# Optimization experiments

Measured on AMD Instinct MI355X. Metric: run time of the kernel, lower is better.

The kernel has to match this reference:

```python
import jax, jax.numpy as jnp
import numpy as np

D = 768      # hidden_size
H = 12       # num_head
HD = D // H  # head_dim
LN_EPS = 1e-5


def setup_inputs() -> dict:
    key = jax.random.key(0)
    ks = jax.random.split(key, 9)
    N, S = 4, 2048
    s = 0.02
    return {
        "hidden_state": jax.random.normal(ks[0], (N, S, D), dtype=jnp.float32),
        "key_padding_mask": jax.random.randint(ks[1], (N, S), 0, 2, dtype=jnp.int64),
        "Wq": jax.random.normal(ks[2], (D, D), dtype=jnp.float32) * s,
        "Wk": jax.random.normal(ks[3], (D, D), dtype=jnp.float32) * s,
        "Wv": jax.random.normal(ks[4], (D, D), dtype=jnp.float32) * s,
        "Wo": jax.random.normal(ks[5], (D, D), dtype=jnp.float32) * s,
        "W1": jax.random.normal(ks[6], (4 * D, D), dtype=jnp.float32) * s,
        "W2": jax.random.normal(ks[7], (D, 4 * D), dtype=jnp.float32) * s,
        "ln_g": jnp.ones((D,), dtype=jnp.float32),
        "ln_b": jnp.zeros((D,), dtype=jnp.float32),
    }


def _layernorm(x, g, b):
    mu = jnp.mean(x, axis=-1, keepdims=True)
    var = jnp.mean(jnp.square(x - mu), axis=-1, keepdims=True)
    return (x - mu) * jax.lax.rsqrt(var + LN_EPS) * g + b


def reference(hidden_state, key_padding_mask, Wq, Wk, Wv, Wo, W1, W2, ln_g, ln_b):
    x = hidden_state
    N, S, _ = x.shape
    # Note: original module projects K and V from `query` (self-attention).
    def proj(W):
        return (x @ W.T).reshape(N, S, H, HD).transpose(0, 2, 1, 3)  # [N,H,S,HD]
    Q, K, V = proj(Wq), proj(Wk), proj(Wv)
    scores = jnp.einsum("bhqd,bhkd->bhqk", Q, K)  # [N,H,S,S]
    # int mask: 0 marks padding positions -> masked with -inf
    pad = (key_padding_mask == 0)[:, None, None, :]  # [N,1,1,S]
    scores = jnp.where(pad, -jnp.inf, scores)
    attn = jax.nn.softmax(scores / np.sqrt(HD), axis=-1)
    ctx = jnp.einsum("bhqk,bhkd->bhqd", attn, V)
    ctx = ctx.transpose(0, 2, 1, 3).reshape(N, S, D)
    mha = ctx @ Wo.T
    # residual + LayerNorm (same LN params used twice, as in the original)
    n1 = _layernorm(x + mha, ln_g, ln_b)
    # FFN with exact GELU (torch nn.GELU default)
    f = jax.nn.gelu(n1 @ W1.T, approximate=False) @ W2.T
    return _layernorm(n1 + f, ln_g, ln_b)
```

## Files before the change

kernel.cpp:

```cpp
#include <hip/hip_runtime.h>
#include <math.h>

typedef unsigned short u16;
typedef unsigned int u32;
typedef __bf16 bf16x8 __attribute__((ext_vector_type(8)));
typedef float f32x4 __attribute__((ext_vector_type(4)));
typedef u32 u32x4 __attribute__((ext_vector_type(4)));

#define NB 4
#define SS 2048
#define DD 768
#define HH 12
#define HD 64
#define ROWS (NB*SS)

__device__ __forceinline__ u16 f2bf(float f) {
    union { float f; unsigned u; } v; v.f = f;
    unsigned r = v.u + 0x7fffu + ((v.u >> 16) & 1u);
    return (u16)(r >> 16);
}
__device__ __forceinline__ u32 fas(float f) { union { float f; u32 u; } v; v.f = f; return v.u; }

__device__ __forceinline__ void gl_lds16(const void* g, void* l) {
    __builtin_amdgcn_global_load_lds((__attribute__((address_space(1))) void*)(g),
                                     (__attribute__((address_space(3))) void*)(l),
                                     16, 0, 0);
}

__global__ __launch_bounds__(256) void prep_kernel(
        const float* __restrict__ X, const float* __restrict__ Wq,
        const float* __restrict__ Wk, const float* __restrict__ Wv,
        const float* __restrict__ Wo, const float* __restrict__ W1,
        const float* __restrict__ W2, const int* __restrict__ mask,
        u16* __restrict__ Xb, u16* __restrict__ Wqkvb, u16* __restrict__ Wob,
        u16* __restrict__ W1b, u16* __restrict__ W2b, float* __restrict__ mb) {
    const int blk = blockIdx.x, tid = threadIdx.x;
    const float* src; u16* dst; int idx;
    if (blk < 6144)       { src = X;  dst = Xb;               idx = blk * 1024 + tid * 4; }
    else if (blk < 6720)  { src = Wq; dst = Wqkvb;            idx = (blk - 6144) * 1024 + tid * 4; }
    else if (blk < 7296)  { src = Wk; dst = Wqkvb + DD * DD;  idx = (blk - 6720) * 1024 + tid * 4; }
    else if (blk < 7872)  { src = Wv; dst = Wqkvb + 2*DD*DD;  idx = (blk - 7296) * 1024 + tid * 4; }
    else if (blk < 8448)  { src = Wo; dst = Wob;              idx = (blk - 7872) * 1024 + tid * 4; }
    else if (blk < 10752) { src = W1; dst = W1b;              idx = (blk - 8448) * 1024 + tid * 4; }
    else if (blk < 13056) { src = W2; dst = W2b;              idx = (blk - 10752) * 1024 + tid * 4; }
    else {
        int i = (blk - 13056) * 1024 + tid * 4;
        float4 o;
        o.x = mask[i]     == 0 ? -1e30f : 0.0f;
        o.y = mask[i + 1] == 0 ? -1e30f : 0.0f;
        o.z = mask[i + 2] == 0 ? -1e30f : 0.0f;
        o.w = mask[i + 3] == 0 ? -1e30f : 0.0f;
        *(float4*)&mb[i] = o;
        return;
    }
    float4 v = *(const float4*)&src[idx];
    ushort4 o;
    o.x = f2bf(v.x); o.y = f2bf(v.y); o.z = f2bf(v.z); o.w = f2bf(v.w);
    *(ushort4*)&dst[idx] = o;
}

template <int EPI, int BN>
__global__ __launch_bounds__(256) void gemm_bt(const u16* __restrict__ A,
                                               const u16* __restrict__ B,
                                               int M, int N, int K,
                                               void* __restrict__ out,
                                               const void* __restrict__ aux,
                                               u16* __restrict__ Qb,
                                               u16* __restrict__ Kb,
                                               u16* __restrict__ Vb) {
    __shared__ __align__(16) u16 lA[128 * 64];
    __shared__ __align__(16) u16 lB[BN * 64];
    constexpr int MI = (BN == 128) ? 4 : 2;
    const int tid = threadIdx.x;
    const int lane = tid & 63, wave = tid >> 6;
    const int quad = lane >> 4, lc = lane & 15;
    const int xcd = blockIdx.x & 7, loc = blockIdx.x >> 3;
    const int mb = xcd * 8 + (loc & 7), nb = loc >> 3;
    const int m0 = mb * 128, n0 = nb * BN;
    const int wrow = (BN == 128) ? (wave >> 1) * 64 : wave * 32;
    const int wcol = (BN == 128) ? (wave & 1) * 64 : 0;
    const int swz = lc & 7;

    f32x4 acc[MI][4] = {};

    for (int kb = 0; kb < K; kb += 64) {
        __syncthreads();
#pragma unroll
        for (int p0 = 0; p0 < 1024; p0 += 256) {
            int p = p0 + tid, row = p >> 3, cl = (p & 7) ^ (row & 7);
            gl_lds16(A + (size_t)(m0 + row) * K + kb + cl * 8, &lA[(size_t)(p0 + wave * 64) * 8]);
        }
#pragma unroll
        for (int p0 = 0; p0 < BN * 8; p0 += 256) {
            int p = p0 + tid, row = p >> 3, cl = (p & 7) ^ (row & 7);
            gl_lds16(B + (size_t)(n0 + row) * K + kb + cl * 8, &lB[(size_t)(p0 + wave * 64) * 8]);
        }
        __syncthreads();
#pragma unroll
        for (int k2 = 0; k2 < 2; ++k2) {
            bf16x8 af[MI], bfr[4];
#pragma unroll
            for (int t = 0; t < MI; ++t)
                af[t] = *(const bf16x8*)&lA[(wrow + t * 16 + lc) * 64 + ((quad + k2 * 4) ^ swz) * 8];
#pragma unroll
            for (int t = 0; t < 4; ++t)
                bfr[t] = *(const bf16x8*)&lB[(wcol + t * 16 + lc) * 64 + ((quad + k2 * 4) ^ swz) * 8];
#pragma unroll
            for (int mi = 0; mi < MI; ++mi)
#pragma unroll
                for (int ni = 0; ni < 4; ++ni)
                    acc[mi][ni] = __builtin_amdgcn_mfma_f32_16x16x32_bf16(af[mi], bfr[ni],
                                                                         acc[mi][ni], 0, 0, 0);
        }
    }

#pragma unroll
    for (int mi = 0; mi < MI; ++mi) {
#pragma unroll
        for (int r = 0; r < 4; ++r) {
            int m = m0 + wrow + mi * 16 + quad * 4 + r;
#pragma unroll
            for (int ni = 0; ni < 4; ++ni) {
                int n = n0 + wcol + ni * 16 + lc;
                float v = acc[mi][ni][r];
                if constexpr (EPI == 0) {
                    int b = m >> 11, s = m & 2047;
                    int which = n / DD, rem = n - which * DD;
                    int h = rem >> 6, d = rem & 63;
                    u16* dst = which == 0 ? Qb : (which == 1 ? Kb : Vb);
                    dst[((((size_t)b * HH + h) * SS + s) << 6) + d] = f2bf(v);
                } else if constexpr (EPI == 1) {
                    float u = v * fmaf(v * v, 0.035677408f, 0.7978845608f);
                    float e = __builtin_amdgcn_exp2f(u * 2.885390082f);
                    float g = v - v * __builtin_amdgcn_rcpf(e + 1.0f);
                    ((u16*)out)[(size_t)m * N + n] = f2bf(g);
                } else if constexpr (EPI == 2) {
                    ((float*)out)[(size_t)m * N + n] =
                        v + ((const float*)aux)[(size_t)m * N + n];
                } else {
                    ((float*)out)[(size_t)m * N + n] =
                        v + (float)(((const __bf16*)aux)[(size_t)m * N + n]);
                }
            }
        }
    }
}

__global__ __launch_bounds__(256) void transpose_v(const u16* __restrict__ V,
                                                   u16* __restrict__ Vt) {
    __shared__ u16 t[32][33];
    int bh = blockIdx.z;
    int s0 = blockIdx.x * 32, d0 = blockIdx.y * 32;
    const u16* vb = V + (size_t)bh * SS * HD;
    u16* vtb = Vt + (size_t)bh * HD * SS;
    int tx = threadIdx.x & 31, ty = threadIdx.x >> 5;
#pragma unroll
    for (int i = 0; i < 32; i += 8) t[ty + i][tx] = vb[(size_t)(s0 + ty + i) * HD + d0 + tx];
    __syncthreads();
#pragma unroll
    for (int i = 0; i < 32; i += 8) vtb[(size_t)(d0 + ty + i) * SS + s0 + tx] = t[tx][ty + i];
}

__global__ __launch_bounds__(256, 3) void attn_kernel(const u16* __restrict__ Q,
                                                      const u16* __restrict__ K,
                                                      const u16* __restrict__ Vt,
                                                      const float* __restrict__ maskbias,
                                                      u16* __restrict__ Ctx) {
    __shared__ __align__(16) u16 lK[2][4224];
    __shared__ __align__(16) u16 lV[2][4096];
    const int tid = threadIdx.x, lane = tid & 63, wave = tid >> 6;
    const int quad = lane >> 4, lc = lane & 15;
    const int bh = blockIdx.x % (NB * HH);
    const int b = bh / HH, h = bh - b * HH;
    const int q0 = (blockIdx.x / (NB * HH)) * 128;
    const u16* Qg = Q + ((size_t)bh * SS + q0 + wave * 32) * HD;
    const u16* Kg = K + (size_t)bh * SS * HD;
    const u16* Vg = Vt + (size_t)bh * HD * SS;
    const float* mbg = maskbias + b * SS;
    const int sw = lc & 7;

    const int srow = tid >> 3, scl = (tid & 7) ^ (srow & 7);
    const int srow2 = (256 + tid) >> 3, scl2 = (tid & 7) ^ (srow2 & 7);

    auto stage = [&](int bi, int j0) {
        gl_lds16(Kg + (size_t)(j0 + srow) * HD + scl * 8,   &lK[bi][(size_t)(wave * 64) * 8]);
        gl_lds16(Kg + (size_t)(j0 + srow2) * HD + scl2 * 8, &lK[bi][(size_t)(256 + wave * 64) * 8]);
        gl_lds16(Vg + (size_t)srow * SS + j0 + scl * 8,     &lV[bi][(size_t)(wave * 64) * 8]);
        gl_lds16(Vg + (size_t)srow2 * SS + j0 + scl2 * 8,   &lV[bi][(size_t)(256 + wave * 64) * 8]);
        if (lane < 16) gl_lds16(mbg + j0 + lane * 4, &lK[bi][4096]);
    };

    bf16x8 qf[2][2];
#pragma unroll
    for (int mi = 0; mi < 2; ++mi)
#pragma unroll
        for (int k2 = 0; k2 < 2; ++k2)
            qf[mi][k2] = *(const bf16x8*)(Qg + (size_t)(mi * 16 + lc) * HD + k2 * 32 + quad * 8);

    bf16x8 onesf;
#pragma unroll
    for (int i = 0; i < 8; ++i) onesf[i] = (__bf16)1.0f;

    f32x4 oacc[2][4] = {};
    f32x4 lsum[2] = {};

    stage(0, 0);
    for (int t = 0; t < SS / 64; ++t) {
        const int cur = t & 1;
        if (t < SS / 64 - 1) {
            stage(cur ^ 1, (t + 1) * 64);
            __builtin_amdgcn_sched_barrier(0);
            asm volatile("s_waitcnt vmcnt(5)" ::: "memory");
        } else {
            __builtin_amdgcn_sched_barrier(0);
            asm volatile("s_waitcnt vmcnt(0)" ::: "memory");
        }
        __builtin_amdgcn_sched_barrier(0);
        __builtin_amdgcn_s_barrier();
        __builtin_amdgcn_sched_barrier(0);

        const u16* bK = &lK[cur][0];
        const u16* bV = &lV[cur][0];
        const float* bM = (const float*)&lK[cur][4096];

        f32x4 sacc[2][4] = {};
        __builtin_amdgcn_s_setprio(1);
#pragma unroll
        for (int k2 = 0; k2 < 2; ++k2) {
            bf16x8 kf[4];
#pragma unroll
            for (int ni = 0; ni < 4; ++ni)
                kf[ni] = *(const bf16x8*)&bK[(ni * 16 + lc) * 64 + ((quad + k2 * 4) ^ sw) * 8];
#pragma unroll
            for (int ni = 0; ni < 4; ++ni) {
                sacc[0][ni] = __builtin_amdgcn_mfma_f32_16x16x32_bf16(kf[ni], qf[0][k2], sacc[0][ni], 0, 0, 0);
                sacc[1][ni] = __builtin_amdgcn_mfma_f32_16x16x32_bf16(kf[ni], qf[1][k2], sacc[1][ni], 0, 0, 0);
            }
        }
        __builtin_amdgcn_s_setprio(0);

        u32 pa[2][4], pb[2][4];
#pragma unroll
        for (int ni = 0; ni < 4; ++ni) {
            f32x4 mbv = *(const f32x4*)&bM[ni * 16 + quad * 4];
#pragma unroll
            for (int mi = 0; mi < 2; ++mi) {
#pragma unroll
                for (int r = 0; r < 4; ++r)
                    sacc[mi][ni][r] = __builtin_amdgcn_exp2f(fmaf(sacc[mi][ni][r], 0.180336880f, mbv[r]));
                pa[mi][ni] = __builtin_amdgcn_perm(fas(sacc[mi][ni][1]), fas(sacc[mi][ni][0]), 0x07060302);
                pb[mi][ni] = __builtin_amdgcn_perm(fas(sacc[mi][ni][3]), fas(sacc[mi][ni][2]), 0x07060302);
            }
        }

        bf16x8 pf[2][2];
#pragma unroll
        for (int mi = 0; mi < 2; ++mi)
#pragma unroll
            for (int k2 = 0; k2 < 2; ++k2) {
                u32 xa = pa[mi][2 * k2], ya = pa[mi][2 * k2 + 1];
                u32 xb = pb[mi][2 * k2], yb = pb[mi][2 * k2 + 1];
                asm("v_permlane32_swap_b32 %0, %1" : "+v"(xa), "+v"(ya));
                asm("v_permlane16_swap_b32 %0, %1" : "+v"(xa), "+v"(ya));
                asm("v_permlane32_swap_b32 %0, %1" : "+v"(xb), "+v"(yb));
                asm("v_permlane16_swap_b32 %0, %1" : "+v"(xb), "+v"(yb));
                u32x4 pw = { xa, xb, ya, yb };
                pf[mi][k2] = __builtin_bit_cast(bf16x8, pw);
            }

        __builtin_amdgcn_s_setprio(1);
#pragma unroll
        for (int k2 = 0; k2 < 2; ++k2) {
            lsum[0] = __builtin_amdgcn_mfma_f32_16x16x32_bf16(pf[0][k2], onesf, lsum[0], 0, 0, 0);
            lsum[1] = __builtin_amdgcn_mfma_f32_16x16x32_bf16(pf[1][k2], onesf, lsum[1], 0, 0, 0);
#pragma unroll
            for (int ni = 0; ni < 4; ++ni) {
                bf16x8 vf = *(const bf16x8*)&bV[(ni * 16 + lc) * 64 + ((quad + k2 * 4) ^ sw) * 8];
                oacc[0][ni] = __builtin_amdgcn_mfma_f32_16x16x32_bf16(pf[0][k2], vf, oacc[0][ni], 0, 0, 0);
                oacc[1][ni] = __builtin_amdgcn_mfma_f32_16x16x32_bf16(pf[1][k2], vf, oacc[1][ni], 0, 0, 0);
            }
        }
        __builtin_amdgcn_s_setprio(0);

        __builtin_amdgcn_sched_barrier(0);
        __builtin_amdgcn_s_barrier();
    }

#pragma unroll
    for (int mi = 0; mi < 2; ++mi)
#pragma unroll
        for (int r = 0; r < 4; ++r) {
            float inv = 1.0f / lsum[mi][r];
            int s = q0 + wave * 32 + mi * 16 + quad * 4 + r;
            size_t base = ((size_t)(b * SS + s)) * DD + h * HD;
#pragma unroll
            for (int ni = 0; ni < 4; ++ni)
                Ctx[base + ni * 16 + lc] = f2bf(oacc[mi][ni][r] * inv);
        }
}

__global__ __launch_bounds__(256) void ln_kernel(const float* __restrict__ in,
                                                 const float* __restrict__ g,
                                                 const float* __restrict__ bb,
                                                 u16* __restrict__ out_bf,
                                                 float* __restrict__ out_f) {
    const int row = blockIdx.x, tid = threadIdx.x;
    const float* x = in + (size_t)row * DD;
    float v0 = x[tid], v1 = x[tid + 256], v2 = x[tid + 512];
    float s = v0 + v1 + v2;
    float q = v0 * v0 + v1 * v1 + v2 * v2;
#pragma unroll
    for (int o = 1; o < 64; o <<= 1) {
        s += __shfl_xor(s, o);
        q += __shfl_xor(q, o);
    }
    __shared__ float rs[4], rq[4];
    int wave = tid >> 6;
    if ((tid & 63) == 0) { rs[wave] = s; rq[wave] = q; }
    __syncthreads();
    s = rs[0] + rs[1] + rs[2] + rs[3];
    q = rq[0] + rq[1] + rq[2] + rq[3];
    float mu = s * (1.0f / DD);
    float var = q * (1.0f / DD) - mu * mu;
    float rstd = rsqrtf(var + 1e-5f);
#pragma unroll
    for (int j = 0; j < 3; ++j) {
        int col = tid + j * 256;
        float v = (j == 0 ? v0 : (j == 1 ? v1 : v2));
        float y = (v - mu) * rstd * g[col] + bb[col];
        if (out_bf) out_bf[(size_t)row * DD + col] = f2bf(y);
        if (out_f) out_f[(size_t)row * DD + col] = y;
    }
}

extern "C" void kernel_launch(void* const* d_in, const int* in_sizes, int n_in,
                              void* d_out, int out_size, void* d_ws, size_t ws_size,
                              hipStream_t stream) {
    const float* X    = (const float*)d_in[0];
    const int*   mask = (const int*)d_in[1];
    const float* Wq   = (const float*)d_in[2];
    const float* Wk   = (const float*)d_in[3];
    const float* Wv   = (const float*)d_in[4];
    const float* Wo   = (const float*)d_in[5];
    const float* W1   = (const float*)d_in[6];
    const float* W2   = (const float*)d_in[7];
    const float* ln_g = (const float*)d_in[8];
    const float* ln_b = (const float*)d_in[9];
    float* out = (float*)d_out;

    char* ws = (char*)d_ws;
    size_t off = 0;
    auto alloc = [&](size_t bytes) {
        void* p = ws + off;
        off += (bytes + 255) & ~(size_t)255;
        return p;
    };
    u16*   Xbf   = (u16*)alloc((size_t)ROWS * DD * 2);
    u16*   Wqkvb = (u16*)alloc((size_t)3 * DD * DD * 2);
    u16*   Wob   = (u16*)alloc((size_t)DD * DD * 2);
    u16*   W1b   = (u16*)alloc((size_t)4 * DD * DD * 2);
    u16*   W2b   = (u16*)alloc((size_t)4 * DD * DD * 2);
    float* mbias = (float*)alloc((size_t)NB * SS * 4);
    u16*   Qb    = (u16*)alloc((size_t)ROWS * DD * 2);
    u16*   Kb    = (u16*)alloc((size_t)ROWS * DD * 2);
    u16*   Vb    = (u16*)alloc((size_t)ROWS * DD * 2);
    u16*   Vtb   = (u16*)alloc((size_t)ROWS * DD * 2);
    float* resid = (float*)alloc((size_t)ROWS * DD * 4);
    u16*   n1b   = (u16*)alloc((size_t)ROWS * DD * 2);
    u16*   Gb    = Qb;
    u16*   Ctxb  = Xbf;
    float* h2    = resid;

    prep_kernel<<<dim3(13064), dim3(256), 0, stream>>>(
        X, Wq, Wk, Wv, Wo, W1, W2, mask,
        Xbf, Wqkvb, Wob, W1b, W2b, mbias);

    gemm_bt<0, 128><<<dim3((3 * DD / 128) * (ROWS / 128)), dim3(256), 0, stream>>>(
        Xbf, Wqkvb, ROWS, 3 * DD, DD, nullptr, nullptr, Qb, Kb, Vb);

    transpose_v<<<dim3(SS / 32, HD / 32, NB * HH), dim3(256), 0, stream>>>(Vb, Vtb);

    attn_kernel<<<dim3((SS / 128) * (NB * HH)), dim3(256), 0, stream>>>(
        Qb, Kb, Vtb, mbias, Ctxb);

    gemm_bt<2, 64><<<dim3((DD / 64) * (ROWS / 128)), dim3(256), 0, stream>>>(
        Ctxb, Wob, ROWS, DD, DD, resid, X, nullptr, nullptr, nullptr);

    ln_kernel<<<dim3(ROWS), dim3(256), 0, stream>>>(resid, ln_g, ln_b, n1b, nullptr);

    gemm_bt<1, 128><<<dim3((4 * DD / 128) * (ROWS / 128)), dim3(256), 0, stream>>>(
        n1b, W1b, ROWS, 4 * DD, DD, Gb, nullptr, nullptr, nullptr, nullptr);

    gemm_bt<3, 64><<<dim3((DD / 64) * (ROWS / 128)), dim3(256), 0, stream>>>(
        Gb, W2b, ROWS, DD, 4 * DD, h2, n1b, nullptr, nullptr, nullptr);

    ln_kernel<<<dim3(ROWS), dim3(256), 0, stream>>>(h2, ln_g, ln_b, nullptr, out);
}
```

Measured before the change: 354.4 us.

## Compact unmasked keys/values and skip padded key tiles in attention

Adds a per-batch prefix-scan kernel over the key padding mask that assigns compacted indices to non-padded positions. The QKV GEMM epilogue scatters K and V rows into these compacted slots, transpose_v skips tiles past the valid count, and attention loops only over ceil(count/64) key tiles, zeroing probabilities in the final partial tile. This removes the additive mask-bias loads and roughly halves attention work for a random 50% mask. It is an exact reformulation, at the cost of a small extra kernel and a scattered epilogue write.

```diff
diff --git a/kernel.cpp b/kernel.cpp
--- a/kernel.cpp
+++ b/kernel.cpp
@@ -31,9 +31,9 @@
         const float* __restrict__ X, const float* __restrict__ Wq,
         const float* __restrict__ Wk, const float* __restrict__ Wv,
         const float* __restrict__ Wo, const float* __restrict__ W1,
-        const float* __restrict__ W2, const int* __restrict__ mask,
+        const float* __restrict__ W2,
         u16* __restrict__ Xb, u16* __restrict__ Wqkvb, u16* __restrict__ Wob,
-        u16* __restrict__ W1b, u16* __restrict__ W2b, float* __restrict__ mb) {
+        u16* __restrict__ W1b, u16* __restrict__ W2b) {
     const int blk = blockIdx.x, tid = threadIdx.x;
     const float* src; u16* dst; int idx;
     if (blk < 6144)       { src = X;  dst = Xb;               idx = blk * 1024 + tid * 4; }
@@ -42,21 +42,45 @@
     else if (blk < 7872)  { src = Wv; dst = Wqkvb + 2*DD*DD;  idx = (blk - 7296) * 1024 + tid * 4; }
     else if (blk < 8448)  { src = Wo; dst = Wob;              idx = (blk - 7872) * 1024 + tid * 4; }
     else if (blk < 10752) { src = W1; dst = W1b;              idx = (blk - 8448) * 1024 + tid * 4; }
-    else if (blk < 13056) { src = W2; dst = W2b;              idx = (blk - 10752) * 1024 + tid * 4; }
-    else {
-        int i = (blk - 13056) * 1024 + tid * 4;
-        float4 o;
-        o.x = mask[i]     == 0 ? -1e30f : 0.0f;
-        o.y = mask[i + 1] == 0 ? -1e30f : 0.0f;
-        o.z = mask[i + 2] == 0 ? -1e30f : 0.0f;
-        o.w = mask[i + 3] == 0 ? -1e30f : 0.0f;
-        *(float4*)&mb[i] = o;
-        return;
-    }
+    else                  { src = W2; dst = W2b;              idx = (blk - 10752) * 1024 + tid * 4; }
     float4 v = *(const float4*)&src[idx];
     ushort4 o;
     o.x = f2bf(v.x); o.y = f2bf(v.y); o.z = f2bf(v.z); o.w = f2bf(v.w);
     *(ushort4*)&dst[idx] = o;
+}
+
+__global__ __launch_bounds__(256) void scan_kernel(const int* __restrict__ mask,
+                                                   int* __restrict__ cidx,
+                                                   int* __restrict__ cnt) {
+    const int b = blockIdx.x, tid = threadIdx.x;
+    const int lane = tid & 63, wave = tid >> 6;
+    const int base = b * SS + tid * 8;
+    int4 m0 = *(const int4*)&mask[base];
+    int4 m1 = *(const int4*)&mask[base + 4];
+    int v[8] = { m0.x != 0, m0.y != 0, m0.z != 0, m0.w != 0,
+                 m1.x != 0, m1.y != 0, m1.z != 0, m1.w != 0 };
+    int own = 0;
+#pragma unroll
+    for (int i = 0; i < 8; ++i) own += v[i];
+    int inc = own;
+#pragma unroll
+    for (int o = 1; o < 64; o <<= 1) {
+        int n = __shfl_up(inc, o);
+        if (lane >= o) inc += n;
+    }
+    __shared__ int wsum[4];
+    if (lane == 63) wsum[wave] = inc;
+    __syncthreads();
+    int wbase = 0;
+#pragma unroll
+    for (int w = 0; w < 4; ++w) wbase += (w < wave) ? wsum[w] : 0;
+    int pos = wbase + inc - own;
+    int o8[8];
+#pragma unroll
+    for (int i = 0; i < 8; ++i) { o8[i] = v[i] ? pos : -1; pos += v[i]; }
+    *(int4*)&cidx[base]     = make_int4(o8[0], o8[1], o8[2], o8[3]);
+    *(int4*)&cidx[base + 4] = make_int4(o8[4], o8[5], o8[6], o8[7]);
+    if (tid == 255) cnt[b] = wbase + inc;
 }
 
 template <int EPI, int BN>
@@ -67,7 +91,8 @@
                                                const void* __restrict__ aux,
                                                u16* __restrict__ Qb,
                                                u16* __restrict__ Kb,
-                                               u16* __restrict__ Vb) {
+                                               u16* __restrict__ Vb,
+                                               const int* __restrict__ cidx) {
     __shared__ __align__(16) u16 lA[128 * 64];
     __shared__ __align__(16) u16 lB[BN * 64];
     constexpr int MI = (BN == 128) ? 4 : 2;
@@ -116,6 +141,12 @@
 
 #pragma unroll
     for (int mi = 0; mi < MI; ++mi) {
+        int csa[4];
+        if constexpr (EPI == 0) {
+            int mbase = m0 + wrow + mi * 16 + quad * 4;
+            int4 cs4 = *(const int4*)&cidx[(mbase >> 11) * SS + (mbase & 2047)];
+            csa[0] = cs4.x; csa[1] = cs4.y; csa[2] = cs4.z; csa[3] = cs4.w;
+        }
 #pragma unroll
         for (int r = 0; r < 4; ++r) {
             int m = m0 + wrow + mi * 16 + quad * 4 + r;
@@ -128,7 +159,9 @@
                     int which = n / DD, rem = n - which * DD;
                     int h = rem >> 6, d = rem & 63;
                     u16* dst = which == 0 ? Qb : (which == 1 ? Kb : Vb);
-                    dst[((((size_t)b * HH + h) * SS + s) << 6) + d] = f2bf(v);
+                    int sidx = which == 0 ? s : csa[r];
+                    if (sidx >= 0)
+                        dst[((((size_t)b * HH + h) * SS + sidx) << 6) + d] = f2bf(v);
                 } else if constexpr (EPI == 1) {
                     float u = v * fmaf(v * v, 0.035677408f, 0.7978845608f);
                     float e = __builtin_amdgcn_exp2f(u * 2.885390082f);
@@ -147,15 +180,22 @@
 }
 
 __global__ __launch_bounds__(256) void transpose_v(const u16* __restrict__ V,
-                                                   u16* __restrict__ Vt) {
+                                                   u16* __restrict__ Vt,
+                                                   const int* __restrict__ cnt) {
     __shared__ u16 t[32][33];
     int bh = blockIdx.z;
+    int c = cnt[bh / HH];
+    int cr = (c + 63) & ~63;
     int s0 = blockIdx.x * 32, d0 = blockIdx.y * 32;
+    if (s0 >= cr) return;
     const u16* vb = V + (size_t)bh * SS * HD;
     u16* vtb = Vt + (size_t)bh * HD * SS;
     int tx = threadIdx.x & 31, ty = threadIdx.x >> 5;
 #pragma unroll
-    for (int i = 0; i < 32; i += 8) t[ty + i][tx] = vb[(size_t)(s0 + ty + i) * HD + d0 + tx];
+    for (int i = 0; i < 32; i += 8) {
+        int s = s0 + ty + i;
+        t[ty + i][tx] = (s < c) ? vb[(size_t)s * HD + d0 + tx] : (u16)0;
+    }
     __syncthreads();
 #pragma unroll
     for (int i = 0; i < 32; i += 8) vtb[(size_t)(d0 + ty + i) * SS + s0 + tx] = t[tx][ty + i];
@@ -164,9 +204,9 @@
 __global__ __launch_bounds__(256, 3) void attn_kernel(const u16* __restrict__ Q,
                                                       const u16* __restrict__ K,
                                                       const u16* __restrict__ Vt,
-                                                      const float* __restrict__ maskbias,
+                                                      const int* __restrict__ cntg,
                                                       u16* __restrict__ Ctx) {
-    __shared__ __align__(16) u16 lK[2][4224];
+    __shared__ __align__(16) u16 lK[2][4096];
     __shared__ __align__(16) u16 lV[2][4096];
     const int tid = threadIdx.x, lane = tid & 63, wave = tid >> 6;
     const int quad = lane >> 4, lc = lane & 15;
@@ -176,8 +216,9 @@
     const u16* Qg = Q + ((size_t)bh * SS + q0 + wave * 32) * HD;
     const u16* Kg = K + (size_t)bh * SS * HD;
     const u16* Vg = Vt + (size_t)bh * HD * SS;
-    const float* mbg = maskbias + b * SS;
     const int sw = lc & 7;
+    const int cnt = cntg[b];
+    const int nt = (cnt + 63) >> 6;
 
     const int srow = tid >> 3, scl = (tid & 7) ^ (srow & 7);
     const int srow2 = (256 + tid) >> 3, scl2 = (tid & 7) ^ (srow2 & 7);
@@ -187,7 +228,6 @@
         gl_lds16(Kg + (size_t)(j0 + srow2) * HD + scl2 * 8, &lK[bi][(size_t)(256 + wave * 64) * 8]);
         gl_lds16(Vg + (size_t)srow * SS + j0 + scl * 8,     &lV[bi][(size_t)(wave * 64) * 8]);
         gl_lds16(Vg + (size_t)srow2 * SS + j0 + scl2 * 8,   &lV[bi][(size_t)(256 + wave * 64) * 8]);
-        if (lane < 16) gl_lds16(mbg + j0 + lane * 4, &lK[bi][4096]);
     };
 
     bf16x8 qf[2][2];
@@ -205,12 +245,12 @@
     f32x4 lsum[2] = {};
 
     stage(0, 0);
-    for (int t = 0; t < SS / 64; ++t) {
+    for (int t = 0; t < nt; ++t) {
         const int cur = t & 1;
-        if (t < SS / 64 - 1) {
+        if (t < nt - 1) {
             stage(cur ^ 1, (t + 1) * 64);
             __builtin_amdgcn_sched_barrier(0);
-            asm volatile("s_waitcnt vmcnt(5)" ::: "memory");
+            asm volatile("s_waitcnt vmcnt(4)" ::: "memory");
         } else {
             __builtin_amdgcn_sched_barrier(0);
             asm volatile("s_waitcnt vmcnt(0)" ::: "memory");
@@ -221,7 +261,6 @@
 
         const u16* bK = &lK[cur][0];
         const u16* bV = &lV[cur][0];
-        const float* bM = (const float*)&lK[cur][4096];
 
         f32x4 sacc[2][4] = {};
         __builtin_amdgcn_s_setprio(1);
@@ -239,15 +278,19 @@
         }
         __builtin_amdgcn_s_setprio(0);
 
+        const int kb_ = cnt - t * 64;
+        const bool part = kb_ < 64;
         u32 pa[2][4], pb[2][4];
 #pragma unroll
         for (int ni = 0; ni < 4; ++ni) {
-            f32x4 mbv = *(const f32x4*)&bM[ni * 16 + quad * 4];
 #pragma unroll
             for (int mi = 0; mi < 2; ++mi) {
 #pragma unroll
-                for (int r = 0; r < 4; ++r)
-                    sacc[mi][ni][r] = __builtin_amdgcn_exp2f(fmaf(sacc[mi][ni][r], 0.180336880f, mbv[r]));
+                for (int r = 0; r < 4; ++r) {
+                    float e = __builtin_amdgcn_exp2f(sacc[mi][ni][r] * 0.180336880f);
+                    if (part) e = (ni * 16 + quad * 4 + r < kb_) ? e : 0.0f;
+                    sacc[mi][ni][r] = e;
+                }
                 pa[mi][ni] = __builtin_amdgcn_perm(fas(sacc[mi][ni][1]), fas(sacc[mi][ni][0]), 0x07060302);
                 pb[mi][ni] = __builtin_amdgcn_perm(fas(sacc[mi][ni][3]), fas(sacc[mi][ni][2]), 0x07060302);
             }
@@ -360,7 +403,8 @@
     u16*   Wob   = (u16*)alloc((size_t)DD * DD * 2);
     u16*   W1b   = (u16*)alloc((size_t)4 * DD * DD * 2);
     u16*   W2b   = (u16*)alloc((size_t)4 * DD * DD * 2);
-    float* mbias = (float*)alloc((size_t)NB * SS * 4);
+    int*   cidx  = (int*)alloc((size_t)NB * SS * 4);
+    int*   cnt   = (int*)alloc(256);
     u16*   Qb    = (u16*)alloc((size_t)ROWS * DD * 2);
     u16*   Kb    = (u16*)alloc((size_t)ROWS * DD * 2);
     u16*   Vb    = (u16*)alloc((size_t)ROWS * DD * 2);
@@ -371,28 +415,30 @@
     u16*   Ctxb  = Xbf;
     float* h2    = resid;
 
-    prep_kernel<<<dim3(13064), dim3(256), 0, stream>>>(
-        X, Wq, Wk, Wv, Wo, W1, W2, mask,
-        Xbf, Wqkvb, Wob, W1b, W2b, mbias);
+    prep_kernel<<<dim3(13056), dim3(256), 0, stream>>>(
+        X, Wq, Wk, Wv, Wo, W1, W2,
+        Xbf, Wqkvb, Wob, W1b, W2b);
+
+    scan_kernel<<<dim3(NB), dim3(256), 0, stream>>>(mask, cidx, cnt);
 
     gemm_bt<0, 128><<<dim3((3 * DD / 128) * (ROWS / 128)), dim3(256), 0, stream>>>(
-        Xbf, Wqkvb, ROWS, 3 * DD, DD, nullptr, nullptr, Qb, Kb, Vb);
-
-    transpose_v<<<dim3(SS / 32, HD / 32, NB * HH), dim3(256), 0, stream>>>(Vb, Vtb);
+        Xbf, Wqkvb, ROWS, 3 * DD, DD, nullptr, nullptr, Qb, Kb, Vb, cidx);
+
+    transpose_v<<<dim3(SS / 32, HD / 32, NB * HH), dim3(256), 0, stream>>>(Vb, Vtb, cnt);
 
     attn_kernel<<<dim3((SS / 128) * (NB * HH)), dim3(256), 0, stream>>>(
-        Qb, Kb, Vtb, mbias, Ctxb);
+        Qb, Kb, Vtb, cnt, Ctxb);
 
     gemm_bt<2, 64><<<dim3((DD / 64) * (ROWS / 128)), dim3(256), 0, stream>>>(
-        Ctxb, Wob, ROWS, DD, DD, resid, X, nullptr, nullptr, nullptr);
+        Ctxb, Wob, ROWS, DD, DD, resid, X, nullptr, nullptr, nullptr, nullptr);
 
     ln_kernel<<<dim3(ROWS), dim3(256), 0, stream>>>(resid, ln_g, ln_b, n1b, nullptr);
 
     gemm_bt<1, 128><<<dim3((4 * DD / 128) * (ROWS / 128)), dim3(256), 0, stream>>>(
-        n1b, W1b, ROWS, 4 * DD, DD, Gb, nullptr, nullptr, nullptr, nullptr);
+        n1b, W1b, ROWS, 4 * DD, DD, Gb, nullptr, nullptr, nullptr, nullptr, nullptr);
 
     gemm_bt<3, 64><<<dim3((DD / 64) * (ROWS / 128)), dim3(256), 0, stream>>>(
-        Gb, W2b, ROWS, DD, 4 * DD, h2, n1b, nullptr, nullptr, nullptr);
+        Gb, W2b, ROWS, DD, 4 * DD, h2, n1b, nullptr, nullptr, nullptr, nullptr);
 
     ln_kernel<<<dim3(ROWS), dim3(256), 0, stream>>>(h2, ln_g, ln_b, nullptr, out);
 }
```

Result: faster. 337.3 us (-4.8%).
